# Optimization experiments

Hardware: AMD Instinct MI355X
Metric: run time of the kernel (lower is better)

## Reference

```python
import jax, jax.numpy as jnp
import numpy as np

ALPHA = 2.0  # ATan surrogate alpha (spikingjelly default)
V_TH = 1.0   # v_threshold
H = 8        # num_heads

@jax.custom_vjp
def atan_spike(x):
    # heaviside(v - v_th); x = v - v_th
    return (x >= 0.0).astype(x.dtype)

def _spike_fwd(x):
    return atan_spike(x), x

def _spike_bwd(x, g):
    pi_half = jnp.asarray(np.pi / 2, x.dtype)
    grad = (ALPHA / 2.0) / (1.0 + (pi_half * ALPHA * x) ** 2)
    return (g * grad,)

atan_spike.defvjp(_spike_fwd, _spike_bwd)

def lif(x_seq, w):
    # MultiStepParametricLIFNode: recurrence over leading dim of x_seq.
    # v <- v + (x - (v - v_reset)) * sigmoid(w); v_reset = 0; hard reset, detach_reset=True.
    sg = jax.nn.sigmoid(w)
    def step(v, x):
        h = v + (x - v) * sg
        s = atan_spike(h - V_TH)
        v_new = h * (1.0 - jax.lax.stop_gradient(s))  # hard reset to 0, detached spike
        return v_new, s
    v0 = jnp.zeros_like(x_seq[0])
    _, spikes = jax.lax.scan(step, v0, x_seq)
    return spikes


def setup_inputs() -> dict:
    key = jax.random.key(0)
    ks = jax.random.split(key, 6)
    T, B, N, C = 4, 32, 196, 512
    s = 0.02
    return {
        "x": jax.random.normal(ks[0], (T, B, N, C), dtype=jnp.float32),
        "Wq": jax.random.normal(ks[1], (C, C), dtype=jnp.float32) * s,
        "Wk": jax.random.normal(ks[2], (C, C), dtype=jnp.float32) * s,
        "Wv": jax.random.normal(ks[3], (C, C), dtype=jnp.float32) * s,
        "Wp": jax.random.normal(ks[4], (C, C), dtype=jnp.float32) * s,
        "bp": jax.random.normal(ks[5], (C,), dtype=jnp.float32) * s,
        "wq": jnp.zeros((), jnp.float32),  # init_tau=2 -> w=0
        "wk": jnp.zeros((), jnp.float32),
        "wv": jnp.zeros((), jnp.float32),
        "wa": jnp.zeros((), jnp.float32),
        "wp": jnp.zeros((), jnp.float32),
    }


def reference(x, Wq, Wk, Wv, Wp, bp, wq, wk, wv, wa, wp):
    T, B, N, C = x.shape
    d = C // H
    scale = d ** (-0.5)
    xf = x.reshape(T * B, N, C)  # LIF steps over T*B (faithful to original flatten(0,1))

    def qkv(W, w_lif):
        y = lif(xf @ W.T, w_lif)                       # [T*B, N, C] binary spikes
        return y.reshape(T, B, N, H, d).transpose(0, 1, 3, 2, 4)  # [T,B,H,N,d]

    q = qkv(Wq, wq)
    k = qkv(Wk, wk)
    v = qkv(Wv, wv)

    attn = jnp.einsum('tbhnd,tbhmd->tbhnm', q, k) * scale   # softmax-free
    y = jnp.einsum('tbhnm,tbhmd->tbhnd', attn, v)           # [T,B,H,N,d]
    y = y.swapaxes(3, 4).reshape(T, B, N, C)                # faithful transpose(3,4).reshape

    y = lif(y, wa)                                          # attn_lif steps over T
    out = lif(y.reshape(T * B, N, C) @ Wp.T + bp, wp)       # proj_lif steps over T*B
    return out.reshape(T, B, N, C)
```

## Files before the change

kernel.cpp:

```cpp
#include <hip/hip_runtime.h>
#include <hip/hip_bf16.h>

#define NC 100352
#define BNC 3211264
typedef unsigned long long ull;

template <bool BIAS>
__global__ __launch_bounds__(256) void gemm_nt(const float* __restrict__ A,
                                               const float* __restrict__ W,
                                               const float* __restrict__ bias,
                                               float* __restrict__ C) {
    __shared__ float As[16][132];
    __shared__ float Bs[16][132];
    const int tid = threadIdx.x;
    const int bm = blockIdx.y * 128;
    const int bn = blockIdx.x * 128;
    const int r0 = tid >> 2;
    const int kq = (tid & 3) << 2;
    const int rg = (tid >> 4) << 2;
    const int cg = (tid & 15) << 2;

    float acc[8][8] = {};
    const float* A0 = A + (size_t)(bm + r0) * 512 + kq;
    const float* A1 = A0 + (size_t)64 * 512;
    const float* W0 = W + (size_t)(bn + r0) * 512 + kq;
    const float* W1 = W0 + (size_t)64 * 512;

    for (int k0 = 0; k0 < 512; k0 += 16) {
        const float4 a0 = *(const float4*)(A0 + k0);
        const float4 a1 = *(const float4*)(A1 + k0);
        const float4 b0 = *(const float4*)(W0 + k0);
        const float4 b1 = *(const float4*)(W1 + k0);
        __syncthreads();
        As[kq + 0][r0] = a0.x; As[kq + 1][r0] = a0.y; As[kq + 2][r0] = a0.z; As[kq + 3][r0] = a0.w;
        As[kq + 0][r0 + 64] = a1.x; As[kq + 1][r0 + 64] = a1.y; As[kq + 2][r0 + 64] = a1.z; As[kq + 3][r0 + 64] = a1.w;
        Bs[kq + 0][r0] = b0.x; Bs[kq + 1][r0] = b0.y; Bs[kq + 2][r0] = b0.z; Bs[kq + 3][r0] = b0.w;
        Bs[kq + 0][r0 + 64] = b1.x; Bs[kq + 1][r0 + 64] = b1.y; Bs[kq + 2][r0 + 64] = b1.z; Bs[kq + 3][r0 + 64] = b1.w;
        __syncthreads();
#pragma unroll
        for (int k = 0; k < 16; ++k) {
            float av[8], bv[8];
            *(float4*)&av[0] = *(const float4*)&As[k][rg];
            *(float4*)&av[4] = *(const float4*)&As[k][rg + 64];
            *(float4*)&bv[0] = *(const float4*)&Bs[k][cg];
            *(float4*)&bv[4] = *(const float4*)&Bs[k][cg + 64];
#pragma unroll
            for (int i = 0; i < 8; ++i)
#pragma unroll
                for (int j = 0; j < 8; ++j)
                    acc[i][j] = fmaf(av[i], bv[j], acc[i][j]);
        }
    }

#pragma unroll
    for (int ih = 0; ih < 2; ++ih)
#pragma unroll
        for (int i = 0; i < 4; ++i) {
            const int row = bm + rg + i + ih * 64;
#pragma unroll
            for (int jh = 0; jh < 2; ++jh) {
                const int col = bn + cg + jh * 64;
                float4 o;
                o.x = acc[ih * 4 + i][jh * 4 + 0];
                o.y = acc[ih * 4 + i][jh * 4 + 1];
                o.z = acc[ih * 4 + i][jh * 4 + 2];
                o.w = acc[ih * 4 + i][jh * 4 + 3];
                if (BIAS) {
                    o.x += bias[col + 0]; o.y += bias[col + 1];
                    o.z += bias[col + 2]; o.w += bias[col + 3];
                }
                *(float4*)&C[(size_t)row * 512 + col] = o;
            }
        }
}

template <int MODE>
__global__ __launch_bounds__(256) void lif_seq(const float* __restrict__ U,
                                               float* __restrict__ S,
                                               ull* __restrict__ M,
                                               const float* __restrict__ wptr,
                                               int steps, int stride) {
    const int i = blockIdx.x * 256 + threadIdx.x;
    if (i >= stride) return;
    const float sg = 1.0f / (1.0f + expf(-wptr[0]));
    const int widx = ((i >> 6) & 7) * 196 + (i >> 9);
    float v = 0.0f;
    for (int t = 0; t < steps; ++t) {
        const float x = U[(size_t)t * stride + i];
        const float h = __fadd_rn(v, __fmul_rn(__fsub_rn(x, v), sg));
        const bool sp = (h >= 1.0f);
        if (MODE == 0) {
            S[(size_t)t * stride + i] = sp ? 1.0f : 0.0f;
        } else {
            const ull m = __ballot(sp);
            if ((threadIdx.x & 63) == 0) M[(size_t)t * 1568 + widx] = m;
        }
        v = sp ? 0.0f : h;
    }
}

__global__ __launch_bounds__(256) void attn_kernel(const ull* __restrict__ Qm,
                                                   const ull* __restrict__ Km,
                                                   const ull* __restrict__ Vm,
                                                   float* __restrict__ Y) {
    const int tb = blockIdx.x >> 3;
    const int h = blockIdx.x & 7;
    const int tid = threadIdx.x;
    const int w = tid >> 6;
    const int lane = tid & 63;

    __shared__ ull qrow[256], krow[256], vrow[256];
    __shared__ ull kcol[64][5], vcol[64][5];
    __shared__ ushort G[64][64];
    __shared__ ushort ybuf[196][66];

    const size_t mb = (size_t)tb * 1568 + (size_t)h * 196;
    if (tid < 196) {
        qrow[tid] = Qm[mb + tid];
        krow[tid] = Km[mb + tid];
        vrow[tid] = Vm[mb + tid];
    } else {
        qrow[tid] = 0; krow[tid] = 0; vrow[tid] = 0;
    }
    __syncthreads();

    {
        ull kc = 0, vc = 0;
#pragma unroll 8
        for (int m = 0; m < 64; ++m) {
            kc |= ((krow[w * 64 + m] >> lane) & 1ull) << m;
            vc |= ((vrow[w * 64 + m] >> lane) & 1ull) << m;
        }
        kcol[lane][w] = kc; vcol[lane][w] = vc;
    }
    __syncthreads();

    for (int p = tid; p < 4096; p += 256) {
        const int d1 = p >> 6, d2 = p & 63;
        const int g = __popcll(kcol[d1][0] & vcol[d2][0]) +
                      __popcll(kcol[d1][1] & vcol[d2][1]) +
                      __popcll(kcol[d1][2] & vcol[d2][2]) +
                      __popcll(kcol[d1][3] & vcol[d2][3]);
        G[d1][d2] = (ushort)g;
    }
    __syncthreads();

    {
        int r = 49 * w;
        const int rend = r + 49;
        for (; r + 1 < rend; r += 2) {
            const ull q0 = qrow[r], q1 = qrow[r + 1];
            const uint a0 = (uint)q0, a1 = (uint)(q0 >> 32);
            const uint b0 = (uint)q1, b1 = (uint)(q1 >> 32);
            uint s0 = 0, s1 = 0;
#pragma unroll
            for (int d = 0; d < 32; ++d) {
                const uint g = G[d][lane];
                s0 += ((a0 >> d) & 1u) * g;
                s1 += ((b0 >> d) & 1u) * g;
            }
#pragma unroll
            for (int d = 0; d < 32; ++d) {
                const uint g = G[32 + d][lane];
                s0 += ((a1 >> d) & 1u) * g;
                s1 += ((b1 >> d) & 1u) * g;
            }
            ybuf[r][lane] = (ushort)s0;
            ybuf[r + 1][lane] = (ushort)s1;
        }
        {
            const ull q0 = qrow[r];
            const uint a0 = (uint)q0, a1 = (uint)(q0 >> 32);
            uint s0 = 0;
#pragma unroll
            for (int d = 0; d < 32; ++d) s0 += ((a0 >> d) & 1u) * (uint)G[d][lane];
#pragma unroll
            for (int d = 0; d < 32; ++d) s0 += ((a1 >> d) & 1u) * (uint)G[32 + d][lane];
            ybuf[r][lane] = (ushort)s0;
        }
    }
    __syncthreads();

    const size_t yb = (size_t)tb * NC + (size_t)h * 12544;
    for (int f = tid; f < 12544; f += 256) {
        const int e = f / 196;
        const int r = f - e * 196;
        Y[yb + f] = (float)ybuf[r][e] * 0.125f;
    }
}

extern "C" void kernel_launch(void* const* d_in, const int* in_sizes, int n_in,
                              void* d_out, int out_size, void* d_ws, size_t ws_size,
                              hipStream_t stream) {
    const float* x  = (const float*)d_in[0];
    const float* Wq = (const float*)d_in[1];
    const float* Wk = (const float*)d_in[2];
    const float* Wv = (const float*)d_in[3];
    const float* Wp = (const float*)d_in[4];
    const float* bp = (const float*)d_in[5];
    const float* wq = (const float*)d_in[6];
    const float* wk = (const float*)d_in[7];
    const float* wv = (const float*)d_in[8];
    const float* wa = (const float*)d_in[9];
    const float* wp = (const float*)d_in[10];
    float* out = (float*)d_out;

    char* ws = (char*)d_ws;
    float* u  = (float*)ws;
    ull* Qm   = (ull*)(ws + 51380224);
    ull* Km   = (ull*)(ws + 51380224 + (size_t)1 * 1605632);
    ull* Vm   = (ull*)(ws + 51380224 + (size_t)2 * 1605632);
    float* ySc = (float*)(ws + 51380224 + (size_t)3 * 1605632);

    const dim3 gGemm(4, 196);
    const dim3 b256(256);

    gemm_nt<false><<<gGemm, b256, 0, stream>>>(x, Wq, nullptr, u);
    lif_seq<1><<<392, 256, 0, stream>>>(u, nullptr, Qm, wq, 128, NC);
    gemm_nt<false><<<gGemm, b256, 0, stream>>>(x, Wk, nullptr, u);
    lif_seq<1><<<392, 256, 0, stream>>>(u, nullptr, Km, wk, 128, NC);
    gemm_nt<false><<<gGemm, b256, 0, stream>>>(x, Wv, nullptr, u);
    lif_seq<1><<<392, 256, 0, stream>>>(u, nullptr, Vm, wv, 128, NC);

    attn_kernel<<<1024, 256, 0, stream>>>(Qm, Km, Vm, ySc);

    lif_seq<0><<<12544, 256, 0, stream>>>(ySc, ySc, nullptr, wa, 4, BNC);

    gemm_nt<true><<<gGemm, b256, 0, stream>>>(ySc, Wp, bp, u);
    lif_seq<0><<<392, 256, 0, stream>>>(u, out, nullptr, wp, 128, NC);
}
```

Measured before the change: 1.012 ms.

## Fuse LIF recurrences into GEMM epilogues and attention, merging QKV into one launch

```diff
diff --git a/kernel.cpp b/kernel.cpp
--- a/kernel.cpp
+++ b/kernel.cpp
@@ -2,108 +2,151 @@
 #include <hip/hip_bf16.h>
 
 #define NC 100352
-#define BNC 3211264
 typedef unsigned long long ull;
-
-template <bool BIAS>
-__global__ __launch_bounds__(256) void gemm_nt(const float* __restrict__ A,
-                                               const float* __restrict__ W,
-                                               const float* __restrict__ bias,
-                                               float* __restrict__ C) {
-    __shared__ float As[16][132];
-    __shared__ float Bs[16][132];
+typedef float (*tile_t)[132];
+
+template <bool PROJ>
+__global__ __launch_bounds__(256) void gemm_lif(
+    const float* __restrict__ A,
+    const float* __restrict__ W0, const float* __restrict__ W1,
+    const float* __restrict__ W2, const float* __restrict__ bias,
+    const float* __restrict__ w0, const float* __restrict__ w1,
+    const float* __restrict__ w2,
+    ull* __restrict__ M, float* __restrict__ out)
+{
+    __shared__ float U[128][132];
+    tile_t As0 = (tile_t)&U[0][0];
+    tile_t As1 = (tile_t)&U[16][0];
+    tile_t Bs0 = (tile_t)&U[32][0];
+    tile_t Bs1 = (tile_t)&U[48][0];
+
+    const int bid = blockIdx.x;
+    int n, cb, br;
+    if (PROJ) {
+        const int work = (bid & 7) * 98 + (bid >> 3);
+        n = work >> 2; cb = work & 3; br = 0;
+    } else {
+        const int work = (bid & 7) * 294 + (bid >> 3);
+        n = work / 12; const int r12 = work - n * 12;
+        br = r12 >> 2; cb = r12 & 3;
+    }
+    const float* Wb   = PROJ ? W0 : (br == 0 ? W0 : (br == 1 ? W1 : W2));
+    const float* wsel = PROJ ? w0 : (br == 0 ? w0 : (br == 1 ? w1 : w2));
+
     const int tid = threadIdx.x;
-    const int bm = blockIdx.y * 128;
-    const int bn = blockIdx.x * 128;
     const int r0 = tid >> 2;
     const int kq = (tid & 3) << 2;
     const int rg = (tid >> 4) << 2;
     const int cg = (tid & 15) << 2;
 
+    const float* Ap0 = A + (size_t)r0 * NC + n * 512 + kq;
+    const float* Ap1 = Ap0 + (size_t)64 * NC;
+    const float* Wq0 = Wb + (size_t)(cb * 128 + r0) * 512 + kq;
+    const float* Wq1 = Wq0 + (size_t)64 * 512;
+
     float acc[8][8] = {};
-    const float* A0 = A + (size_t)(bm + r0) * 512 + kq;
-    const float* A1 = A0 + (size_t)64 * 512;
-    const float* W0 = W + (size_t)(bn + r0) * 512 + kq;
-    const float* W1 = W0 + (size_t)64 * 512;
-
-    for (int k0 = 0; k0 < 512; k0 += 16) {
-        const float4 a0 = *(const float4*)(A0 + k0);
-        const float4 a1 = *(const float4*)(A1 + k0);
-        const float4 b0 = *(const float4*)(W0 + k0);
-        const float4 b1 = *(const float4*)(W1 + k0);
-        __syncthreads();
-        As[kq + 0][r0] = a0.x; As[kq + 1][r0] = a0.y; As[kq + 2][r0] = a0.z; As[kq + 3][r0] = a0.w;
-        As[kq + 0][r0 + 64] = a1.x; As[kq + 1][r0 + 64] = a1.y; As[kq + 2][r0 + 64] = a1.z; As[kq + 3][r0 + 64] = a1.w;
-        Bs[kq + 0][r0] = b0.x; Bs[kq + 1][r0] = b0.y; Bs[kq + 2][r0] = b0.z; Bs[kq + 3][r0] = b0.w;
-        Bs[kq + 0][r0 + 64] = b1.x; Bs[kq + 1][r0 + 64] = b1.y; Bs[kq + 2][r0 + 64] = b1.z; Bs[kq + 3][r0 + 64] = b1.w;
-        __syncthreads();
+    float4 sa0, sa1, sb0, sb1;
+
+    auto LOAD = [&](int k) {
+        sa0 = *(const float4*)(Ap0 + k);
+        sa1 = *(const float4*)(Ap1 + k);
+        sb0 = *(const float4*)(Wq0 + k);
+        sb1 = *(const float4*)(Wq1 + k);
+    };
+    auto STORE = [&](tile_t A_, tile_t B_) {
+        A_[kq + 0][r0] = sa0.x; A_[kq + 1][r0] = sa0.y;
+        A_[kq + 2][r0] = sa0.z; A_[kq + 3][r0] = sa0.w;
+        A_[kq + 0][r0 + 64] = sa1.x; A_[kq + 1][r0 + 64] = sa1.y;
+        A_[kq + 2][r0 + 64] = sa1.z; A_[kq + 3][r0 + 64] = sa1.w;
+        B_[kq + 0][r0] = sb0.x; B_[kq + 1][r0] = sb0.y;
+        B_[kq + 2][r0] = sb0.z; B_[kq + 3][r0] = sb0.w;
+        B_[kq + 0][r0 + 64] = sb1.x; B_[kq + 1][r0 + 64] = sb1.y;
+        B_[kq + 2][r0 + 64] = sb1.z; B_[kq + 3][r0 + 64] = sb1.w;
+    };
+    auto COMP = [&](const tile_t A_, const tile_t B_) {
 #pragma unroll
         for (int k = 0; k < 16; ++k) {
             float av[8], bv[8];
-            *(float4*)&av[0] = *(const float4*)&As[k][rg];
-            *(float4*)&av[4] = *(const float4*)&As[k][rg + 64];
-            *(float4*)&bv[0] = *(const float4*)&Bs[k][cg];
-            *(float4*)&bv[4] = *(const float4*)&Bs[k][cg + 64];
+            *(float4*)&av[0] = *(const float4*)&A_[k][rg];
+            *(float4*)&av[4] = *(const float4*)&A_[k][rg + 64];
+            *(float4*)&bv[0] = *(const float4*)&B_[k][cg];
+            *(float4*)&bv[4] = *(const float4*)&B_[k][cg + 64];
 #pragma unroll
             for (int i = 0; i < 8; ++i)
 #pragma unroll
                 for (int j = 0; j < 8; ++j)
                     acc[i][j] = fmaf(av[i], bv[j], acc[i][j]);
         }
+    };
+
+    LOAD(0); STORE(As0, Bs0);
+    __syncthreads();
+    for (int kk = 0; kk < 512; kk += 32) {
+        LOAD(kk + 16);
+        COMP(As0, Bs0);
+        STORE(As1, Bs1);
+        __syncthreads();
+        if (kk + 32 < 512) {
+            LOAD(kk + 32);
+            COMP(As1, Bs1);
+            STORE(As0, Bs0);
+        } else {
+            COMP(As1, Bs1);
+        }
+        __syncthreads();
     }
 
 #pragma unroll
     for (int ih = 0; ih < 2; ++ih)
 #pragma unroll
         for (int i = 0; i < 4; ++i) {
-            const int row = bm + rg + i + ih * 64;
+            const int row = rg + i + ih * 64;
 #pragma unroll
             for (int jh = 0; jh < 2; ++jh) {
-                const int col = bn + cg + jh * 64;
                 float4 o;
                 o.x = acc[ih * 4 + i][jh * 4 + 0];
                 o.y = acc[ih * 4 + i][jh * 4 + 1];
                 o.z = acc[ih * 4 + i][jh * 4 + 2];
                 o.w = acc[ih * 4 + i][jh * 4 + 3];
-                if (BIAS) {
-                    o.x += bias[col + 0]; o.y += bias[col + 1];
-                    o.z += bias[col + 2]; o.w += bias[col + 3];
+                if (PROJ) {
+                    const int colb = cb * 128 + cg + jh * 64;
+                    o.x += bias[colb + 0]; o.y += bias[colb + 1];
+                    o.z += bias[colb + 2]; o.w += bias[colb + 3];
                 }
-                *(float4*)&C[(size_t)row * 512 + col] = o;
-            }
-        }
+                *(float4*)&U[row][cg + jh * 64] = o;
+            }
+        }
+    __syncthreads();
+
+    if (tid < 128) {
+        const float sg = 1.0f / (1.0f + expf(-wsel[0]));
+        const int c = tid, lane = tid & 63;
+        const int hglob = cb * 2 + (c >> 6);
+        ull* Mw = M + (size_t)br * 200704 + (size_t)hglob * 196 + n;
+        float* Ow = out + (size_t)n * 512 + cb * 128 + c;
+        float v = 0.0f;
+        for (int tb = 0; tb < 128; ++tb) {
+            const float uu = U[tb][c];
+            const float hh = __fadd_rn(v, __fmul_rn(__fsub_rn(uu, v), sg));
+            const bool sp = hh >= 1.0f;
+            if (PROJ) {
+                Ow[(size_t)tb * NC] = sp ? 1.0f : 0.0f;
+            } else {
+                const ull mm = __ballot(sp);
+                if (lane == 0) Mw[(size_t)tb * 1568] = mm;
+            }
+            v = sp ? 0.0f : hh;
+        }
+    }
 }
 
-template <int MODE>
-__global__ __launch_bounds__(256) void lif_seq(const float* __restrict__ U,
-                                               float* __restrict__ S,
-                                               ull* __restrict__ M,
-                                               const float* __restrict__ wptr,
-                                               int steps, int stride) {
-    const int i = blockIdx.x * 256 + threadIdx.x;
-    if (i >= stride) return;
-    const float sg = 1.0f / (1.0f + expf(-wptr[0]));
-    const int widx = ((i >> 6) & 7) * 196 + (i >> 9);
-    float v = 0.0f;
-    for (int t = 0; t < steps; ++t) {
-        const float x = U[(size_t)t * stride + i];
-        const float h = __fadd_rn(v, __fmul_rn(__fsub_rn(x, v), sg));
-        const bool sp = (h >= 1.0f);
-        if (MODE == 0) {
-            S[(size_t)t * stride + i] = sp ? 1.0f : 0.0f;
-        } else {
-            const ull m = __ballot(sp);
-            if ((threadIdx.x & 63) == 0) M[(size_t)t * 1568 + widx] = m;
-        }
-        v = sp ? 0.0f : h;
-    }
-}
-
-__global__ __launch_bounds__(256) void attn_kernel(const ull* __restrict__ Qm,
-                                                   const ull* __restrict__ Km,
-                                                   const ull* __restrict__ Vm,
-                                                   float* __restrict__ Y) {
-    const int tb = blockIdx.x >> 3;
+__global__ __launch_bounds__(256) void attn_fused(const ull* __restrict__ Qm,
+                                                  const ull* __restrict__ Km,
+                                                  const ull* __restrict__ Vm,
+                                                  const float* __restrict__ wa,
+                                                  float* __restrict__ Y)
+{
+    const int b = blockIdx.x >> 3;
     const int h = blockIdx.x & 7;
     const int tid = threadIdx.x;
     const int w = tid >> 6;
@@ -112,80 +155,104 @@
     __shared__ ull qrow[256], krow[256], vrow[256];
     __shared__ ull kcol[64][5], vcol[64][5];
     __shared__ ushort G[64][64];
-    __shared__ ushort ybuf[196][66];
-
-    const size_t mb = (size_t)tb * 1568 + (size_t)h * 196;
-    if (tid < 196) {
-        qrow[tid] = Qm[mb + tid];
-        krow[tid] = Km[mb + tid];
-        vrow[tid] = Vm[mb + tid];
-    } else {
-        qrow[tid] = 0; krow[tid] = 0; vrow[tid] = 0;
-    }
-    __syncthreads();
-
-    {
-        ull kc = 0, vc = 0;
+    __shared__ float vstate[196][64];
+    __shared__ ull sbm[208];
+
+    const float sg = 1.0f / (1.0f + expf(-wa[0]));
+
+    for (int t = 0; t < 4; ++t) {
+        const int tb = t * 32 + b;
+        const size_t mb = (size_t)tb * 1568 + (size_t)h * 196;
+        if (tid < 196) {
+            qrow[tid] = Qm[mb + tid];
+            krow[tid] = Km[mb + tid];
+            vrow[tid] = Vm[mb + tid];
+        } else {
+            qrow[tid] = 0; krow[tid] = 0; vrow[tid] = 0;
+        }
+        __syncthreads();
+
+        {
+            ull kc = 0, vc = 0;
 #pragma unroll 8
-        for (int m = 0; m < 64; ++m) {
-            kc |= ((krow[w * 64 + m] >> lane) & 1ull) << m;
-            vc |= ((vrow[w * 64 + m] >> lane) & 1ull) << m;
-        }
-        kcol[lane][w] = kc; vcol[lane][w] = vc;
-    }
-    __syncthreads();
-
-    for (int p = tid; p < 4096; p += 256) {
-        const int d1 = p >> 6, d2 = p & 63;
-        const int g = __popcll(kcol[d1][0] & vcol[d2][0]) +
-                      __popcll(kcol[d1][1] & vcol[d2][1]) +
-                      __popcll(kcol[d1][2] & vcol[d2][2]) +
-                      __popcll(kcol[d1][3] & vcol[d2][3]);
-        G[d1][d2] = (ushort)g;
-    }
-    __syncthreads();
-
-    {
-        int r = 49 * w;
-        const int rend = r + 49;
-        for (; r + 1 < rend; r += 2) {
-            const ull q0 = qrow[r], q1 = qrow[r + 1];
-            const uint a0 = (uint)q0, a1 = (uint)(q0 >> 32);
-            const uint b0 = (uint)q1, b1 = (uint)(q1 >> 32);
-            uint s0 = 0, s1 = 0;
-#pragma unroll
-            for (int d = 0; d < 32; ++d) {
-                const uint g = G[d][lane];
-                s0 += ((a0 >> d) & 1u) * g;
-                s1 += ((b0 >> d) & 1u) * g;
-            }
-#pragma unroll
-            for (int d = 0; d < 32; ++d) {
-                const uint g = G[32 + d][lane];
-                s0 += ((a1 >> d) & 1u) * g;
-                s1 += ((b1 >> d) & 1u) * g;
-            }
-            ybuf[r][lane] = (ushort)s0;
-            ybuf[r + 1][lane] = (ushort)s1;
-        }
+            for (int m = 0; m < 64; ++m) {
+                kc |= ((krow[w * 64 + m] >> lane) & 1ull) << m;
+                vc |= ((vrow[w * 64 + m] >> lane) & 1ull) << m;
+            }
+            kcol[lane][w] = kc; vcol[lane][w] = vc;
+        }
+        __syncthreads();
+
+        for (int p = tid; p < 4096; p += 256) {
+            const int d1 = p >> 6, d2 = p & 63;
+            const int g = __popcll(kcol[d1][0] & vcol[d2][0]) +
+                          __popcll(kcol[d1][1] & vcol[d2][1]) +
+                          __popcll(kcol[d1][2] & vcol[d2][2]) +
+                          __popcll(kcol[d1][3] & vcol[d2][3]);
+            G[d1][d2] = (ushort)g;
+        }
+        __syncthreads();
+
         {
-            const ull q0 = qrow[r];
-            const uint a0 = (uint)q0, a1 = (uint)(q0 >> 32);
-            uint s0 = 0;
-#pragma unroll
-            for (int d = 0; d < 32; ++d) s0 += ((a0 >> d) & 1u) * (uint)G[d][lane];
-#pragma unroll
-            for (int d = 0; d < 32; ++d) s0 += ((a1 >> d) & 1u) * (uint)G[32 + d][lane];
-            ybuf[r][lane] = (ushort)s0;
-        }
-    }
-    __syncthreads();
-
-    const size_t yb = (size_t)tb * NC + (size_t)h * 12544;
-    for (int f = tid; f < 12544; f += 256) {
-        const int e = f / 196;
-        const int r = f - e * 196;
-        Y[yb + f] = (float)ybuf[r][e] * 0.125f;
+            int r = 49 * w;
+            const int rend = r + 49;
+            for (; r + 1 < rend; r += 2) {
+                const ull q0 = qrow[r], q1 = qrow[r + 1];
+                const uint a0 = (uint)q0, a1 = (uint)(q0 >> 32);
+                const uint b0 = (uint)q1, b1 = (uint)(q1 >> 32);
+                uint s0 = 0, s1 = 0;
+#pragma unroll
+                for (int d = 0; d < 32; ++d) {
+                    const uint g = G[d][lane];
+                    s0 += ((a0 >> d) & 1u) * g;
+                    s1 += ((b0 >> d) & 1u) * g;
+                }
+#pragma unroll
+                for (int d = 0; d < 32; ++d) {
+                    const uint g = G[32 + d][lane];
+                    s0 += ((a1 >> d) & 1u) * g;
+                    s1 += ((b1 >> d) & 1u) * g;
+                }
+                const float y0 = (float)s0 * 0.125f;
+                const float v0 = t ? vstate[r][lane] : 0.0f;
+                const float h0 = __fadd_rn(v0, __fmul_rn(__fsub_rn(y0, v0), sg));
+                const bool sp0 = h0 >= 1.0f;
+                vstate[r][lane] = sp0 ? 0.0f : h0;
+                const ull m0 = __ballot(sp0);
+                const float y1 = (float)s1 * 0.125f;
+                const float v1 = t ? vstate[r + 1][lane] : 0.0f;
+                const float h1 = __fadd_rn(v1, __fmul_rn(__fsub_rn(y1, v1), sg));
+                const bool sp1 = h1 >= 1.0f;
+                vstate[r + 1][lane] = sp1 ? 0.0f : h1;
+                const ull m1 = __ballot(sp1);
+                if (lane == 0) { sbm[r] = m0; sbm[r + 1] = m1; }
+            }
+            {
+                const ull q0 = qrow[r];
+                const uint a0 = (uint)q0, a1 = (uint)(q0 >> 32);
+                uint s0 = 0;
+#pragma unroll
+                for (int d = 0; d < 32; ++d) s0 += ((a0 >> d) & 1u) * (uint)G[d][lane];
+#pragma unroll
+                for (int d = 0; d < 32; ++d) s0 += ((a1 >> d) & 1u) * (uint)G[32 + d][lane];
+                const float y0 = (float)s0 * 0.125f;
+                const float v0 = t ? vstate[r][lane] : 0.0f;
+                const float h0 = __fadd_rn(v0, __fmul_rn(__fsub_rn(y0, v0), sg));
+                const bool sp0 = h0 >= 1.0f;
+                vstate[r][lane] = sp0 ? 0.0f : h0;
+                const ull m0 = __ballot(sp0);
+                if (lane == 0) sbm[r] = m0;
+            }
+        }
+        __syncthreads();
+
+        const size_t yb = (size_t)tb * NC + (size_t)h * 12544;
+        for (int f = tid; f < 12544; f += 256) {
+            const int e = f / 196;
+            const int r2 = f - e * 196;
+            Y[yb + f] = ((sbm[r2] >> e) & 1ull) ? 1.0f : 0.0f;
+        }
+        __syncthreads();
     }
 }
 
@@ -206,26 +273,16 @@
     float* out = (float*)d_out;
 
     char* ws = (char*)d_ws;
-    float* u  = (float*)ws;
-    ull* Qm   = (ull*)(ws + 51380224);
-    ull* Km   = (ull*)(ws + 51380224 + (size_t)1 * 1605632);
-    ull* Vm   = (ull*)(ws + 51380224 + (size_t)2 * 1605632);
-    float* ySc = (float*)(ws + 51380224 + (size_t)3 * 1605632);
-
-    const dim3 gGemm(4, 196);
-    const dim3 b256(256);
-
-    gemm_nt<false><<<gGemm, b256, 0, stream>>>(x, Wq, nullptr, u);
-    lif_seq<1><<<392, 256, 0, stream>>>(u, nullptr, Qm, wq, 128, NC);
-    gemm_nt<false><<<gGemm, b256, 0, stream>>>(x, Wk, nullptr, u);
-    lif_seq<1><<<392, 256, 0, stream>>>(u, nullptr, Km, wk, 128, NC);
-    gemm_nt<false><<<gGemm, b256, 0, stream>>>(x, Wv, nullptr, u);
-    lif_seq<1><<<392, 256, 0, stream>>>(u, nullptr, Vm, wv, 128, NC);
-
-    attn_kernel<<<1024, 256, 0, stream>>>(Qm, Km, Vm, ySc);
-
-    lif_seq<0><<<12544, 256, 0, stream>>>(ySc, ySc, nullptr, wa, 4, BNC);
-
-    gemm_nt<true><<<gGemm, b256, 0, stream>>>(ySc, Wp, bp, u);
-    lif_seq<0><<<392, 256, 0, stream>>>(u, out, nullptr, wp, 128, NC);
+    ull* Qm = (ull*)ws;
+    ull* Km = Qm + 200704;
+    ull* Vm = Km + 200704;
+    float* ySc = (float*)(ws + (size_t)3 * 1605632);
+
+    gemm_lif<false><<<2352, 256, 0, stream>>>(x, Wq, Wk, Wv, nullptr,
+                                              wq, wk, wv, Qm, nullptr);
+
+    attn_fused<<<256, 256, 0, stream>>>(Qm, Km, Vm, wa, ySc);
+
+    gemm_lif<true><<<784, 256, 0, stream>>>(ySc, Wp, nullptr, nullptr, bp,
+                                            wp, nullptr, nullptr, nullptr, out);
 }
```

Result: faster. 955.1 us (-5.6%).
